# Performance work log

Hardware: AMD Instinct MI355X
Metric: run time of the kernel (lower is better)

## Reference

```python
import jax, jax.numpy as jnp
import numpy as np

N = 1536        # nodes in batch
E = 24576       # directed edges (avg in-degree 16)
H_DIM = 128     # hidden_dim
D = 1280        # input_dim (esm embedding size)
K_HOPS = 2
RATIO = 0.5     # node-drop pooling keep ratio
NEG = -1e9

def _leaky(v):
    return jnp.where(v > 0, v, 0.2 * v)

def setup_inputs():
    key = jax.random.key(0)
    ks = jax.random.split(key, 11)
    x = jax.random.normal(ks[0], (N, H_DIM), jnp.float32)
    x_orig = jax.random.normal(ks[1], (N, D), jnp.float32) * 0.1
    edge_index = jax.random.randint(ks[2], (2, E), 0, N, dtype=jnp.int32)
    batch = jnp.zeros((N,), jnp.int32)
    W1 = jax.random.normal(ks[3], (H_DIM, D), jnp.float32) / np.sqrt(H_DIM).astype(np.float32)
    a_src1 = jax.random.normal(ks[4], (D,), jnp.float32) / np.sqrt(D).astype(np.float32)
    a_dst1 = jax.random.normal(ks[5], (D,), jnp.float32) / np.sqrt(D).astype(np.float32)
    b1 = jnp.zeros((D,), jnp.float32)
    w2 = jax.random.normal(ks[6], (D,), jnp.float32) / np.sqrt(D).astype(np.float32)
    a_s2 = jax.random.normal(ks[7], (), jnp.float32)
    a_d2 = jax.random.normal(ks[8], (), jnp.float32)
    b2 = jnp.zeros((), jnp.float32)
    return {"x": x, "x_orig": x_orig, "edge_index": edge_index, "batch": batch,
            "W1": W1, "a_src1": a_src1, "a_dst1": a_dst1, "b1": b1,
            "w2": w2, "a_s2": a_s2, "a_d2": a_d2, "b2": b2}

def _forward(x, x_orig, edge_index, batch, W1, a_src1, a_dst1, b1, w2, a_s2, a_d2, b2):
    n = x.shape[0]
    src, tgt = edge_index[0], edge_index[1]
    sl = jnp.arange(n, dtype=src.dtype)
    src2 = jnp.concatenate([src, sl])   # PyG GATConv adds self-loops
    tgt2 = jnp.concatenate([tgt, sl])

    # ---- conv1: GATConv(hidden_dim -> input_dim, heads=1) on full graph ----
    h = x @ W1                                          # [N, D]
    e = _leaky((h @ a_src1)[src2] + (h @ a_dst1)[tgt2])  # [E+N]
    mx = jax.ops.segment_max(e, tgt2, num_segments=n)
    ex = jnp.exp(e - mx[tgt2])
    den = jax.ops.segment_sum(ex, tgt2, num_segments=n)
    alpha = ex / den[tgt2]
    x_gat = jax.ops.segment_sum(alpha[:, None] * h[src2], tgt2, num_segments=n) + b1

    # ---- batched k-hop ego masks (flow source->target, center included) ----
    A = jnp.zeros((n, n), jnp.float32).at[src, tgt].set(1.0)
    M = jnp.eye(n, dtype=jnp.float32)
    for _ in range(K_HOPS):
        M = jnp.minimum(M + M @ A.T, 1.0)
    Mb = M > 0                                          # [N_ego, N_node]

    # ---- pooling scorer GAT(D->1) on x_sub = x_gat[v] * x_orig[u] ----
    # h2[v,u] = sum_d x_gat[v,d] * x_orig[u,d] * w2[d]
    H2 = (x_gat * w2) @ x_orig.T                        # [N_ego, N_node]
    hs, ht = H2[:, src2], H2[:, tgt2]                   # [N_ego, E+N]
    valid = Mb[:, src2] & Mb[:, tgt2]
    e2 = jnp.where(valid, _leaky(a_s2 * hs + a_d2 * ht), NEG)

    def row(e_row, hs_row):  # attention softmax + aggregate within one ego
        m = jax.ops.segment_max(e_row, tgt2, num_segments=n)
        w = jnp.exp(e_row - m[tgt2])
        d = jax.ops.segment_sum(w, tgt2, num_segments=n)
        nu = jax.ops.segment_sum(w * hs_row, tgt2, num_segments=n)
        return nu / jnp.maximum(d, 1e-12)
    score = jax.vmap(row)(e2, hs) + b2                  # [N_ego, N_node]

    # ---- node-drop pooling: keep top ceil(RATIO*|ego|) nodes per ego ----
    size = jnp.sum(Mb, axis=1).astype(jnp.float32)
    k_keep = jnp.ceil(RATIO * size).astype(jnp.int32)
    score_m = jnp.where(Mb, score, NEG)
    order = jnp.argsort(-score_m, axis=1)
    rank = jnp.argsort(order, axis=1)
    keep = (rank < k_keep[:, None]) & Mb
    out = jnp.where(keep, jax.nn.sigmoid(score), 0.0)   # padded score matrix
    return out, keep

def reference(x, x_orig, edge_index, batch, W1, a_src1, a_dst1, b1, w2, a_s2, a_d2, b2):
    return _forward(x, x_orig, edge_index, batch, W1, a_src1, a_dst1, b1, w2, a_s2, a_d2, b2)
```

## Files before the change

kernel.cpp:

```cpp
#include <hip/hip_runtime.h>
#include <math.h>

#define N 1536
#define E 24576
#define HD 128
#define D 1280
#define NW 24
#define RT 16
#define KSP 2
#define KSL 640

#define NB_SPLIT 1920
#define NB_DEG   102
#define NB_H     480

typedef unsigned long long u64;
typedef unsigned short u16;
typedef unsigned int u32;
typedef __attribute__((ext_vector_type(8))) short bf16x8;
typedef __attribute__((ext_vector_type(4))) float f32x4;

#define GLDS(g, l) __builtin_amdgcn_global_load_lds( \
    (const __attribute__((address_space(1))) unsigned int*)(g), \
    (__attribute__((address_space(3))) unsigned int*)(l), 16, 0, 0)

__device__ __forceinline__ double lrelu(double v){ return v > 0.0 ? v : 0.2*v; }

__device__ __forceinline__ double fexp(double x){
    double n = __builtin_rint(x * 1.4426950408889634);
    double r = __builtin_fma(-n, 0.6931471805599453, x);
    r = __builtin_fma(-n, 2.3190468138462996e-17, r);
    double p = 2.505210838544172e-8;
    p = __builtin_fma(p, r, 2.755731922398589e-7);
    p = __builtin_fma(p, r, 2.7557319223985893e-6);
    p = __builtin_fma(p, r, 2.48015873015873e-5);
    p = __builtin_fma(p, r, 1.984126984126984e-4);
    p = __builtin_fma(p, r, 1.3888888888888889e-3);
    p = __builtin_fma(p, r, 8.333333333333333e-3);
    p = __builtin_fma(p, r, 4.1666666666666664e-2);
    p = __builtin_fma(p, r, 1.6666666666666666e-1);
    p = __builtin_fma(p, r, 0.5);
    p = __builtin_fma(p, r, 1.0);
    p = __builtin_fma(p, r, 1.0);
    long long ni = (long long)n;
    double s = __longlong_as_double((u64)(ni + 1023) << 52);
    return (x < -700.0) ? 0.0 : p * s;
}

__device__ __forceinline__ float fexpf_(float x){
    float n = __builtin_rintf(x * 1.44269504f);
    float r = __builtin_fmaf(-n, 0.693359375f, x);
    r = __builtin_fmaf(-n, -2.12194440e-4f, r);
    float p = 1.9841270e-4f;
    p = __builtin_fmaf(p, r, 1.3888889e-3f);
    p = __builtin_fmaf(p, r, 8.3333333e-3f);
    p = __builtin_fmaf(p, r, 4.1666667e-2f);
    p = __builtin_fmaf(p, r, 1.6666667e-1f);
    p = __builtin_fmaf(p, r, 0.5f);
    p = __builtin_fmaf(p, r, 1.0f);
    p = __builtin_fmaf(p, r, 1.0f);
    int ni = (int)n;
    float s = __uint_as_float((u32)(ni + 127) << 23);
    return p * s;
}

__device__ __forceinline__ void bsplit(float f, u16& h, u16& l){
    unsigned u = __float_as_uint(f);
    unsigned hr = (u + 0x7fffu + ((u>>16)&1u)) >> 16;
    h = (u16)hr;
    float hf = __uint_as_float(hr << 16);
    float r = f - hf;
    unsigned u2 = __float_as_uint(r);
    l = (u16)((u2 + 0x7fffu + ((u2>>16)&1u)) >> 16);
}

__global__ void k_prep(const float* __restrict__ xo, u16* __restrict__ Xhi, u16* __restrict__ Xlo,
                       const int* __restrict__ ei, u64* __restrict__ IN, int* __restrict__ deg,
                       const float* __restrict__ x, const float* __restrict__ W1,
                       float* __restrict__ h32){
    int bid = blockIdx.x, tid = threadIdx.x;
    if (bid < NB_SPLIT){
        int idx = (bid*256 + tid)*4;
        float4 v = *(const float4*)&xo[idx];
        ushort4 h, l;
        bsplit(v.x, h.x, l.x); bsplit(v.y, h.y, l.y);
        bsplit(v.z, h.z, l.z); bsplit(v.w, h.w, l.w);
        *(ushort4*)&Xhi[idx] = h;
        *(ushort4*)&Xlo[idx] = l;
    } else if (bid < NB_SPLIT + NB_DEG){
        int idx = (bid - NB_SPLIT)*256 + tid;
        if (idx < E){
            int s = ei[idx], t = ei[E+idx];
            atomicOr(&IN[(size_t)t*NW + (s>>6)], 1ULL << (s&63));
            atomicAdd(&deg[t], 1);
        } else if (idx < E+N){
            atomicAdd(&deg[idx-E], 1);
        }
    } else {
        int r = bid - (NB_SPLIT + NB_DEG);
        int rb = (r/5)*RT;
        int col = (r%5)*256 + tid;
        __shared__ float xL[RT*HD];
        for (int u=tid; u<RT*HD; u+=256) xL[u] = x[(size_t)rb*HD + u];
        __syncthreads();
        float acc[RT];
        #pragma unroll
        for (int rr=0; rr<RT; rr++) acc[rr] = 0.0f;
        const float* wp = &W1[col];
        #pragma unroll 4
        for (int k=0; k<HD; k++){
            float w = wp[(size_t)k*D];
            #pragma unroll
            for (int rr=0; rr<RT; rr++) acc[rr] = __builtin_fmaf(w, xL[rr*HD + k], acc[rr]);
        }
        #pragma unroll
        for (int rr=0; rr<RT; rr++) h32[(size_t)(rb+rr)*D + col] = acc[rr];
    }
}

__global__ void k_graph(const int* __restrict__ deg, int* __restrict__ coff, int* __restrict__ cursor,
                        const u64* __restrict__ IN, u64* __restrict__ Mb,
                        u16* __restrict__ cols, int* __restrict__ cnt){
    int tid = threadIdx.x;
    if (blockIdx.x == 0){
        __shared__ int ls[256];
        int v[6]; int s = 0;
        for (int u=0; u<6; u++){ v[u] = s; s += deg[tid*6+u]; }
        ls[tid] = s; __syncthreads();
        for (int d=1; d<256; d<<=1){
            int t2 = (tid>=d) ? ls[tid-d] : 0;
            __syncthreads();
            ls[tid] += t2;
            __syncthreads();
        }
        int base = (tid>0) ? ls[tid-1] : 0;
        for (int u=0; u<6; u++){
            int o = base + v[u];
            coff[tid*6+u] = o; cursor[tid*6+u] = o;
        }
        if (tid==255) coff[N] = ls[255];
        return;
    }
    int i = blockIdx.x - 1, ln = tid;
    __shared__ int scn[256];
    __shared__ u16 lst[N];
    u64 b = 0;
    if (ln < NW){
        b = IN[(size_t)i*NW + ln];
        if ((i>>6) == ln) b |= 1ULL << (i&63);
    }
    int pc = (ln < NW) ? __popcll(b) : 0;
    scn[ln] = pc; __syncthreads();
    for (int d=1; d<64; d<<=1){
        int v = (ln>=d) ? scn[ln-d] : 0;
        __syncthreads();
        scn[ln] += v;
        __syncthreads();
    }
    {
        int idx = scn[ln] - pc;
        u64 bb = b;
        while (bb){
            int k = __ffsll((unsigned long long)bb) - 1;
            bb &= bb - 1;
            lst[idx++] = (u16)(ln*64 + k);
        }
    }
    __syncthreads();
    int nn = scn[63];
    u64 R0 = b, R1 = 0, R2 = 0, R3 = 0;
    int u = 0;
    if (ln < NW){
        for (; u+3 < nn; u += 4){
            R0 |= IN[(size_t)lst[u  ]*NW + ln];
            R1 |= IN[(size_t)lst[u+1]*NW + ln];
            R2 |= IN[(size_t)lst[u+2]*NW + ln];
            R3 |= IN[(size_t)lst[u+3]*NW + ln];
        }
        for (; u < nn; u++) R0 |= IN[(size_t)lst[u]*NW + ln];
    }
    u64 R = (R0 | R1) | (R2 | R3);
    if (ln < NW) Mb[(size_t)i*NW + ln] = R;
    __syncthreads();
    pc = (ln < NW) ? __popcll(R) : 0;
    scn[ln] = pc; __syncthreads();
    for (int d=1; d<64; d<<=1){
        int v = (ln>=d) ? scn[ln-d] : 0;
        __syncthreads();
        scn[ln] += v;
        __syncthreads();
    }
    if (ln == 63) cnt[i] = scn[63];
    int idx = scn[ln] - pc;
    u64 bb = R;
    while (bb){
        int k = __ffsll((unsigned long long)bb) - 1;
        bb &= bb - 1;
        cols[(size_t)i*N + idx++] = (u16)(ln*64 + k);
    }
}

__global__ void k_fill_hv(const int* __restrict__ ei, int* __restrict__ cursor, u16* __restrict__ csr_src,
                          const float* __restrict__ h32, const float* __restrict__ as1,
                          const float* __restrict__ ad1, double* __restrict__ hs1,
                          double* __restrict__ hd1){
    int tid = threadIdx.x;
    if (blockIdx.x < NB_DEG){
        int idx = blockIdx.x*256 + tid;
        if (idx < E){
            int s = ei[idx], t = ei[E+idx];
            int p = atomicAdd(&cursor[t], 1);
            csr_src[p] = (u16)s;
        } else if (idx < E+N){
            int t = idx - E;
            int p = atomicAdd(&cursor[t], 1);
            csr_src[p] = (u16)t;
        }
        return;
    }
    int i = blockIdx.x - NB_DEG;
    __shared__ double ra[256], rb[256];
    double a = 0, b = 0;
    for (int d=tid; d<D; d+=256){
        double hv = (double)h32[(size_t)i*D + d];
        a += hv * (double)as1[d];
        b += hv * (double)ad1[d];
    }
    ra[tid] = a; rb[tid] = b; __syncthreads();
    for (int s=128; s>0; s>>=1){
        if (tid < s){ ra[tid] += ra[tid+s]; rb[tid] += rb[tid+s]; }
        __syncthreads();
    }
    if (tid == 0){ hs1[i] = ra[0]; hd1[i] = rb[0]; }
}

__global__ void k_gat(const int* __restrict__ coff, const u16* __restrict__ csr_src,
                      const double* __restrict__ hs1, const double* __restrict__ hd1,
                      const float* __restrict__ h32,
                      const float* __restrict__ b1, const float* __restrict__ w2,
                      u16* __restrict__ Ghi, u16* __restrict__ Glo){
    int t = blockIdx.x, tid = threadIdx.x;
    int o0 = coff[t], o1 = coff[t+1], dg = o1 - o0;
    __shared__ double red[256];
    __shared__ float als[256];
    __shared__ int ssrc[256];
    __shared__ double DD;
    double hdt = hd1[t];
    double dsum = 0.0;
    for (int j=tid; j<dg; j+=256){
        int s = csr_src[o0+j];
        double e = lrelu(hs1[s] + hdt);
        dsum += fexp(e);
    }
    red[tid] = dsum; __syncthreads();
    for (int step=128; step>0; step>>=1){
        if (tid < step) red[tid] += red[tid+step];
        __syncthreads();
    }
    if (tid == 0) DD = red[0];
    __syncthreads();
    double Dv = DD;
    float acc[5] = {0,0,0,0,0};
    for (int base=0; base<dg; base+=256){
        int j = base + tid;
        if (j < dg){
            int s = csr_src[o0+j];
            double e = lrelu(hs1[s] + hdt);
            als[tid] = (float)(fexp(e)/Dv); ssrc[tid] = s;
        }
        __syncthreads();
        int lim = min(256, dg-base);
        for (int u=0; u<lim; u+=2){
            float a0 = als[u];
            int s0 = ssrc[u];
            bool h1 = (u+1 < lim);
            float a1 = h1 ? als[u+1] : 0.0f;
            int s1 = h1 ? ssrc[u+1] : s0;
            const float* hp0 = &h32[(size_t)s0*D];
            const float* hp1 = &h32[(size_t)s1*D];
            #pragma unroll
            for (int q=0; q<5; q++)
                acc[q] = __builtin_fmaf(a1, hp1[tid + 256*q],
                         __builtin_fmaf(a0, hp0[tid + 256*q], acc[q]));
        }
        __syncthreads();
    }
    #pragma unroll
    for (int q=0; q<5; q++){
        int d = tid + 256*q;
        float g = (acc[q] + b1[d]) * w2[d];
        u16 gh, gl;
        bsplit(g, gh, gl);
        Ghi[(size_t)t*D + d] = gh;
        Glo[(size_t)t*D + d] = gl;
    }
}

__global__ __launch_bounds__(512, 4)
void k_h2mm(const u16* __restrict__ Ghi, const u16* __restrict__ Glo,
            const u16* __restrict__ Xhi, const u16* __restrict__ Xlo,
            float* __restrict__ Hp){
    __shared__ u16 S[2*4*4096];
    int tid = threadIdx.x;
    int ks = blockIdx.x & (KSP-1);
    int tile = blockIdx.x >> 1;
    int bm = tile / 12, bn = tile % 12;
    int k0 = ks * KSL;
    int w = tid >> 6, L = tid & 63;
    int sr = w*16 + (L >> 2);
    int sc = (L & 3) * 8;
    size_t gA = (size_t)(bm*128 + sr)*D + k0 + sc;
    size_t gB = (size_t)(bn*128 + sr)*D + k0 + sc;
    int lw = w * 512;
    int l16 = L & 15, qd = L >> 4;
    int wm = (w & 1)*64, wn = (w >> 1)*32;
    f32x4 acc[4][2];
    #pragma unroll
    for (int a=0; a<4; a++)
        #pragma unroll
        for (int b=0; b<2; b++) acc[a][b] = (f32x4){0.f,0.f,0.f,0.f};

    #define STAGE(B, KB) do{ \
        GLDS(Ghi + gA + (KB), S + ((B)*4+0)*4096 + lw); \
        GLDS(Glo + gA + (KB), S + ((B)*4+1)*4096 + lw); \
        GLDS(Xhi + gB + (KB), S + ((B)*4+2)*4096 + lw); \
        GLDS(Xlo + gB + (KB), S + ((B)*4+3)*4096 + lw); \
    }while(0)

    STAGE(0, 0);
    const int NT = KSL/32;
    #pragma unroll 1
    for (int t = 0; t < NT; t++){
        int cur = t & 1;
        if (t+1 < NT){
            STAGE(cur^1, (t+1)*32);
            asm volatile("s_waitcnt vmcnt(4)" ::: "memory");
        } else {
            asm volatile("s_waitcnt vmcnt(0)" ::: "memory");
        }
        __builtin_amdgcn_s_barrier();
        const u16* Ah = S + (cur*4+0)*4096;
        const u16* Al = S + (cur*4+1)*4096;
        const u16* Bh = S + (cur*4+2)*4096;
        const u16* Bl = S + (cur*4+3)*4096;
        bf16x8 ahi[4], alo[4];
        #pragma unroll
        for (int tm=0; tm<4; tm++){
            ahi[tm] = *(const bf16x8*)&Ah[(wm + tm*16 + l16)*32 + qd*8];
            alo[tm] = *(const bf16x8*)&Al[(wm + tm*16 + l16)*32 + qd*8];
        }
        #pragma unroll
        for (int tn=0; tn<2; tn++){
            bf16x8 bhf = *(const bf16x8*)&Bh[(wn + tn*16 + l16)*32 + qd*8];
            bf16x8 blf = *(const bf16x8*)&Bl[(wn + tn*16 + l16)*32 + qd*8];
            #pragma unroll
            for (int tm=0; tm<4; tm++){
                acc[tm][tn] = __builtin_amdgcn_mfma_f32_16x16x32_bf16(ahi[tm], bhf, acc[tm][tn], 0, 0, 0);
                acc[tm][tn] = __builtin_amdgcn_mfma_f32_16x16x32_bf16(alo[tm], bhf, acc[tm][tn], 0, 0, 0);
                acc[tm][tn] = __builtin_amdgcn_mfma_f32_16x16x32_bf16(ahi[tm], blf, acc[tm][tn], 0, 0, 0);
            }
        }
        __builtin_amdgcn_s_barrier();
    }
    #undef STAGE
    float* HO = Hp + (size_t)ks*N*N;
    #pragma unroll
    for (int tm=0; tm<4; tm++){
        int rbase = bm*128 + wm + tm*16 + qd*4;
        #pragma unroll
        for (int tn=0; tn<2; tn++){
            int cg = bn*128 + wn + tn*16 + l16;
            #pragma unroll
            for (int reg=0; reg<4; reg++)
                HO[(size_t)(rbase+reg)*N + cg] = acc[tm][tn][reg];
        }
    }
}

__global__ void k_score_rank(const float* __restrict__ Hp, const u64* __restrict__ Mb,
                             const u16* __restrict__ cols, const int* __restrict__ cnt,
                             const int* __restrict__ coff, const u16* __restrict__ csr_src,
                             const float* __restrict__ pas2, const float* __restrict__ pad2,
                             const float* __restrict__ pb2, float* __restrict__ out){
    int i = blockIdx.x, tid = threadIdx.x;
    __shared__ __align__(16) float HL[N];
    __shared__ u64 MbL[NW];
    __shared__ u16 clL[N];
    __shared__ u64 KL[N];
    __shared__ int hist[256];
    __shared__ u64 sPrefix;
    __shared__ int sKK;
    float* keepO = out + (size_t)N*N;
    {
        const float4* P0 = (const float4*)(Hp + (size_t)i*N);
        const float4* P1 = (const float4*)(Hp + (size_t)N*N + (size_t)i*N);
        float4* H4 = (float4*)HL;
        for (int u=tid; u<N/4; u+=256){
            float4 a=P0[u], b=P1[u];
            float4 r;
            r.x = a.x+b.x; r.y = a.y+b.y; r.z = a.z+b.z; r.w = a.w+b.w;
            H4[u] = r;
        }
    }
    if (tid < NW) MbL[tid] = Mb[(size_t)i*NW + tid];
    __syncthreads();
    float as2 = pas2[0], ad2 = pad2[0];
    double b2 = (double)pb2[0];
    int c0 = cnt[i];
    c0 = min(max(c0, 0), N);
    for (int c=tid; c<c0; c+=256){
        int t = cols[(size_t)i*N + c];
        float ht = HL[t];
        float zd = ad2 * ht;
        int o0 = coff[t], o1 = coff[t+1];
        double den = 0.0, nu = 0.0;
        int p = o0;
        for (; p+7 < o1; p += 8){
            int s[8]; float h[8]; float wv[8];
            #pragma unroll
            for (int q=0; q<8; q++) s[q] = csr_src[p+q];
            #pragma unroll
            for (int q=0; q<8; q++) h[q] = HL[s[q]];
            #pragma unroll
            for (int q=0; q<8; q++){
                bool v = (MbL[s[q]>>6] >> (s[q]&63)) & 1ULL;
                float z = __builtin_fmaf(as2, h[q], zd);
                float e = z > 0.f ? z : 0.2f*z;
                e = fminf(fmaxf(e, -80.f), 80.f);
                wv[q] = v ? fexpf_(e) : 0.0f;
            }
            #pragma unroll
            for (int q=0; q<8; q++){
                den += (double)wv[q];
                nu  += (double)(wv[q]*h[q]);
            }
        }
        for (; p < o1; p++){
            int s = csr_src[p];
            bool v = (MbL[s>>6] >> (s&63)) & 1ULL;
            float hs = HL[s];
            float z = __builtin_fmaf(as2, hs, zd);
            float e = z > 0.0f ? z : 0.2f*z;
            e = fminf(fmaxf(e, -80.0f), 80.0f);
            float w = v ? fexpf_(e) : 0.0f;
            den += (double)w;
            nu  += (double)(w * hs);
        }
        float sf = (float)(nu / fmax(den, 1e-12) + b2);
        clL[c] = (u16)t;
        u32 kb = __float_as_uint(sf);
        kb = (kb & 0x80000000u) ? ~kb : (kb | 0x80000000u);
        KL[c] = ((u64)kb << 16) | (u32)(1535 - t);
    }
    __syncthreads();
    for (int d=tid; d<N; d+=256) HL[d] = 0.0f;
    int k = (c0 + 1) >> 1;
    if (tid == 0){ sPrefix = 0; sKK = k; }
    #pragma unroll 1
    for (int shift = 40; shift >= 0; shift -= 8){
        hist[tid] = 0;
        __syncthreads();
        u64 pref = sPrefix;
        int kkr = sKK;
        for (int c=tid; c<c0; c+=256){
            u64 key = KL[c];
            if ((key >> (shift+8)) == (pref >> (shift+8)))
                atomicAdd(&hist[(int)((key>>shift)&255)], 1);
        }
        __syncthreads();
        if (tid < 64){
            int Lx = tid;
            int b0 = hist[4*Lx], b1v = hist[4*Lx+1], b2v = hist[4*Lx+2], b3v = hist[4*Lx+3];
            int tot = ((b0 + b1v) + (b2v + b3v));
            int run = tot;
            #pragma unroll
            for (int d=1; d<64; d<<=1){
                int o = __shfl_down(run, d);
                if (Lx + d < 64) run += o;
            }
            int after = run - tot;
            int s3 = b3v + after, s2 = b2v + s3, s1 = b1v + s2, s0 = b0 + s1;
            int dg = -1, rem = 0;
            if (s0 >= kkr && s1 < kkr){ dg = 4*Lx;   rem = kkr - s1; }
            else if (s1 >= kkr && s2 < kkr){ dg = 4*Lx+1; rem = kkr - s2; }
            else if (s2 >= kkr && s3 < kkr){ dg = 4*Lx+2; rem = kkr - s3; }
            else if (s3 >= kkr && after < kkr){ dg = 4*Lx+3; rem = kkr - after; }
            if (dg >= 0){
                sPrefix = pref | ((u64)(u32)dg << shift);
                sKK = rem;
            }
        }
        __syncthreads();
    }
    u64 T = sPrefix;
    for (int p=tid; p<c0; p+=256){
        u64 Kp = KL[p];
        if (Kp >= T){
            u32 kb = (u32)(Kp >> 16);
            u32 orig = (kb & 0x80000000u) ? (kb & 0x7fffffffu) : ~kb;
            float sf = __uint_as_float(orig);
            HL[clL[p]] = 1.0f/(1.0f + fexpf_(fminf(fmaxf(-sf,-80.f),80.f)));
        }
    }
    __syncthreads();
    {
        const float4* H4 = (const float4*)HL;
        float4* O0 = (float4*)(out   + (size_t)i*N);
        float4* O1 = (float4*)(keepO + (size_t)i*N);
        for (int u=tid; u<N/4; u+=256){
            float4 s = H4[u];
            float4 kk;
            kk.x = (s.x > 0.0f) ? 1.0f : 0.0f;
            kk.y = (s.y > 0.0f) ? 1.0f : 0.0f;
            kk.z = (s.z > 0.0f) ? 1.0f : 0.0f;
            kk.w = (s.w > 0.0f) ? 1.0f : 0.0f;
            O0[u] = s;
            O1[u] = kk;
        }
    }
}

extern "C" void kernel_launch(void* const* d_in, const int* in_sizes, int n_in,
                              void* d_out, int out_size, void* d_ws, size_t ws_size,
                              hipStream_t stream){
    const float* x   = (const float*)d_in[0];
    const float* xo  = (const float*)d_in[1];
    const int*   ei  = (const int*)  d_in[2];
    const float* W1  = (const float*)d_in[4];
    const float* as1 = (const float*)d_in[5];
    const float* ad1 = (const float*)d_in[6];
    const float* b1  = (const float*)d_in[7];
    const float* w2  = (const float*)d_in[8];
    const float* as2 = (const float*)d_in[9];
    const float* ad2 = (const float*)d_in[10];
    const float* b2  = (const float*)d_in[11];
    float* out = (float*)d_out;

    char* w = (char*)d_ws;
    size_t o = 0;
    auto alloc = [&](size_t b)->char*{ char* r = w + o; o = (o + b + 255) & ~(size_t)255; return r; };

    float*  h32   = (float*) alloc((size_t)N*D*4);
    float*  Hp    = (float*) alloc((size_t)KSP*N*N*4);
    u16*    Ghi   = (u16*)   alloc((size_t)N*D*2);
    u16*    Glo   = (u16*)   alloc((size_t)N*D*2);
    u16*    Xhi   = (u16*)   alloc((size_t)N*D*2);
    u16*    Xlo   = (u16*)   alloc((size_t)N*D*2);
    u64*    IN    = (u64*)   alloc((size_t)N*NW*8);
    int*    deg   = (int*)   alloc((size_t)N*4);
    u64*    Mb    = (u64*)   alloc((size_t)N*NW*8);
    double* hs1   = (double*)alloc((size_t)N*8);
    double* hd1   = (double*)alloc((size_t)N*8);
    int*    coff  = (int*)   alloc((size_t)(N+1)*4);
    int*    cursor= (int*)   alloc((size_t)N*4);
    u16*    csr   = (u16*)   alloc((size_t)(E+N)*2);
    u16*    cols  = (u16*)   alloc((size_t)N*N*2);
    int*    cnt   = (int*)   alloc((size_t)N*4);

    hipMemsetAsync(IN, 0, (size_t)N*NW*8 + (size_t)N*4, stream);

    k_prep   <<<NB_SPLIT + NB_DEG + NB_H, 256, 0, stream>>>(xo, Xhi, Xlo, ei, IN, deg, x, W1, h32);
    k_graph  <<<N + 1, 256, 0, stream>>>(deg, coff, cursor, IN, Mb, cols, cnt);
    k_fill_hv<<<NB_DEG + N, 256, 0, stream>>>(ei, cursor, csr, h32, as1, ad1, hs1, hd1);
    k_gat    <<<N, 256, 0, stream>>>(coff, csr, hs1, hd1, h32, b1, w2, Ghi, Glo);
    k_h2mm   <<<144*KSP, 512, 0, stream>>>(Ghi, Glo, Xhi, Xlo, Hp);
    k_score_rank<<<N, 256, 0, stream>>>(Hp, Mb, cols, cnt, coff, csr, as2, ad2, b2, out);
}
```

Before: 202.7 us.

## Move ego-mask construction into GAT kernel blocks and shrink scan to single block

The 2-hop ego-mask/column-list work moves out of the former graph kernel into extra blocks of the GAT aggregation kernel, which now launches 2N blocks. Shared memory is unioned between the two roles. The degree prefix scan becomes its own one-block kernel. The aim is to shorten the critical path before fill_hv by running the mask work concurrently with GAT aggregation, at the cost of a larger GAT grid and some reshuffled barriers.

```diff
diff --git a/kernel.cpp b/kernel.cpp
--- a/kernel.cpp
+++ b/kernel.cpp
@@ -118,86 +118,24 @@
     }
 }
 
-__global__ void k_graph(const int* __restrict__ deg, int* __restrict__ coff, int* __restrict__ cursor,
-                        const u64* __restrict__ IN, u64* __restrict__ Mb,
-                        u16* __restrict__ cols, int* __restrict__ cnt){
+__global__ void k_scan(const int* __restrict__ deg, int* __restrict__ coff, int* __restrict__ cursor){
+    __shared__ int ls[256];
     int tid = threadIdx.x;
-    if (blockIdx.x == 0){
-        __shared__ int ls[256];
-        int v[6]; int s = 0;
-        for (int u=0; u<6; u++){ v[u] = s; s += deg[tid*6+u]; }
-        ls[tid] = s; __syncthreads();
-        for (int d=1; d<256; d<<=1){
-            int t2 = (tid>=d) ? ls[tid-d] : 0;
-            __syncthreads();
-            ls[tid] += t2;
-            __syncthreads();
-        }
-        int base = (tid>0) ? ls[tid-1] : 0;
-        for (int u=0; u<6; u++){
-            int o = base + v[u];
-            coff[tid*6+u] = o; cursor[tid*6+u] = o;
-        }
-        if (tid==255) coff[N] = ls[255];
-        return;
-    }
-    int i = blockIdx.x - 1, ln = tid;
-    __shared__ int scn[256];
-    __shared__ u16 lst[N];
-    u64 b = 0;
-    if (ln < NW){
-        b = IN[(size_t)i*NW + ln];
-        if ((i>>6) == ln) b |= 1ULL << (i&63);
-    }
-    int pc = (ln < NW) ? __popcll(b) : 0;
-    scn[ln] = pc; __syncthreads();
-    for (int d=1; d<64; d<<=1){
-        int v = (ln>=d) ? scn[ln-d] : 0;
-        __syncthreads();
-        scn[ln] += v;
-        __syncthreads();
-    }
-    {
-        int idx = scn[ln] - pc;
-        u64 bb = b;
-        while (bb){
-            int k = __ffsll((unsigned long long)bb) - 1;
-            bb &= bb - 1;
-            lst[idx++] = (u16)(ln*64 + k);
-        }
-    }
-    __syncthreads();
-    int nn = scn[63];
-    u64 R0 = b, R1 = 0, R2 = 0, R3 = 0;
-    int u = 0;
-    if (ln < NW){
-        for (; u+3 < nn; u += 4){
-            R0 |= IN[(size_t)lst[u  ]*NW + ln];
-            R1 |= IN[(size_t)lst[u+1]*NW + ln];
-            R2 |= IN[(size_t)lst[u+2]*NW + ln];
-            R3 |= IN[(size_t)lst[u+3]*NW + ln];
-        }
-        for (; u < nn; u++) R0 |= IN[(size_t)lst[u]*NW + ln];
-    }
-    u64 R = (R0 | R1) | (R2 | R3);
-    if (ln < NW) Mb[(size_t)i*NW + ln] = R;
-    __syncthreads();
-    pc = (ln < NW) ? __popcll(R) : 0;
-    scn[ln] = pc; __syncthreads();
-    for (int d=1; d<64; d<<=1){
-        int v = (ln>=d) ? scn[ln-d] : 0;
-        __syncthreads();
-        scn[ln] += v;
-        __syncthreads();
-    }
-    if (ln == 63) cnt[i] = scn[63];
-    int idx = scn[ln] - pc;
-    u64 bb = R;
-    while (bb){
-        int k = __ffsll((unsigned long long)bb) - 1;
-        bb &= bb - 1;
-        cols[(size_t)i*N + idx++] = (u16)(ln*64 + k);
-    }
+    int v[6]; int s = 0;
+    for (int u=0; u<6; u++){ v[u] = s; s += deg[tid*6+u]; }
+    ls[tid] = s; __syncthreads();
+    for (int d=1; d<256; d<<=1){
+        int t2 = (tid>=d) ? ls[tid-d] : 0;
+        __syncthreads();
+        ls[tid] += t2;
+        __syncthreads();
+    }
+    int base = (tid>0) ? ls[tid-1] : 0;
+    for (int u=0; u<6; u++){
+        int o = base + v[u];
+        coff[tid*6+u] = o; cursor[tid*6+u] = o;
+    }
+    if (tid==255) coff[N] = ls[255];
 }
 
 __global__ void k_fill_hv(const int* __restrict__ ei, int* __restrict__ cursor, u16* __restrict__ csr_src,
@@ -238,13 +176,74 @@
                       const double* __restrict__ hs1, const double* __restrict__ hd1,
                       const float* __restrict__ h32,
                       const float* __restrict__ b1, const float* __restrict__ w2,
-                      u16* __restrict__ Ghi, u16* __restrict__ Glo){
-    int t = blockIdx.x, tid = threadIdx.x;
+                      u16* __restrict__ Ghi, u16* __restrict__ Glo,
+                      const u64* __restrict__ IN, u64* __restrict__ Mb,
+                      u16* __restrict__ cols, int* __restrict__ cnt){
+    __shared__ union {
+        struct { double red[256]; float als[256]; int ssrc[256]; double DD; } g;
+        struct { int scn[256]; u16 lst[N]; } m;
+    } U;
+    int tid = threadIdx.x;
+    if (blockIdx.x >= N){
+        int i = blockIdx.x - N, ln = tid;
+        u64 b = 0;
+        if (ln < NW){
+            b = IN[(size_t)i*NW + ln];
+            if ((i>>6) == ln) b |= 1ULL << (i&63);
+        }
+        int pc = (ln < NW) ? __popcll(b) : 0;
+        U.m.scn[ln] = pc; __syncthreads();
+        for (int d=1; d<64; d<<=1){
+            int v = (ln>=d) ? U.m.scn[ln-d] : 0;
+            __syncthreads();
+            U.m.scn[ln] += v;
+            __syncthreads();
+        }
+        {
+            int idx = U.m.scn[ln] - pc;
+            u64 bb = b;
+            while (bb){
+                int k = __ffsll((unsigned long long)bb) - 1;
+                bb &= bb - 1;
+                U.m.lst[idx++] = (u16)(ln*64 + k);
+            }
+        }
+        __syncthreads();
+        int nn = U.m.scn[63];
+        u64 R0 = b, R1 = 0, R2 = 0, R3 = 0;
+        int u = 0;
+        if (ln < NW){
+            for (; u+3 < nn; u += 4){
+                R0 |= IN[(size_t)U.m.lst[u  ]*NW + ln];
+                R1 |= IN[(size_t)U.m.lst[u+1]*NW + ln];
+                R2 |= IN[(size_t)U.m.lst[u+2]*NW + ln];
+                R3 |= IN[(size_t)U.m.lst[u+3]*NW + ln];
+            }
+            for (; u < nn; u++) R0 |= IN[(size_t)U.m.lst[u]*NW + ln];
+        }
+        u64 R = (R0 | R1) | (R2 | R3);
+        if (ln < NW) Mb[(size_t)i*NW + ln] = R;
+        __syncthreads();
+        pc = (ln < NW) ? __popcll(R) : 0;
+        U.m.scn[ln] = pc; __syncthreads();
+        for (int d=1; d<64; d<<=1){
+            int v = (ln>=d) ? U.m.scn[ln-d] : 0;
+            __syncthreads();
+            U.m.scn[ln] += v;
+            __syncthreads();
+        }
+        if (ln == 63) cnt[i] = U.m.scn[63];
+        int idx = U.m.scn[ln] - pc;
+        u64 bb = R;
+        while (bb){
+            int k = __ffsll((unsigned long long)bb) - 1;
+            bb &= bb - 1;
+            cols[(size_t)i*N + idx++] = (u16)(ln*64 + k);
+        }
+        return;
+    }
+    int t = blockIdx.x;
     int o0 = coff[t], o1 = coff[t+1], dg = o1 - o0;
-    __shared__ double red[256];
-    __shared__ float als[256];
-    __shared__ int ssrc[256];
-    __shared__ double DD;
     double hdt = hd1[t];
     double dsum = 0.0;
     for (int j=tid; j<dg; j+=256){
@@ -252,30 +251,31 @@
         double e = lrelu(hs1[s] + hdt);
         dsum += fexp(e);
     }
-    red[tid] = dsum; __syncthreads();
+    U.g.red[tid] = dsum; __syncthreads();
     for (int step=128; step>0; step>>=1){
-        if (tid < step) red[tid] += red[tid+step];
-        __syncthreads();
-    }
-    if (tid == 0) DD = red[0];
+        if (tid < step) U.g.red[tid] += U.g.red[tid+step];
+        __syncthreads();
+    }
+    if (tid == 0) U.g.DD = U.g.red[0];
     __syncthreads();
-    double Dv = DD;
+    double Dv = U.g.DD;
     float acc[5] = {0,0,0,0,0};
     for (int base=0; base<dg; base+=256){
         int j = base + tid;
+        __syncthreads();
         if (j < dg){
             int s = csr_src[o0+j];
             double e = lrelu(hs1[s] + hdt);
-            als[tid] = (float)(fexp(e)/Dv); ssrc[tid] = s;
+            U.g.als[tid] = (float)(fexp(e)/Dv); U.g.ssrc[tid] = s;
         }
         __syncthreads();
         int lim = min(256, dg-base);
         for (int u=0; u<lim; u+=2){
-            float a0 = als[u];
-            int s0 = ssrc[u];
+            float a0 = U.g.als[u];
+            int s0 = U.g.ssrc[u];
             bool h1 = (u+1 < lim);
-            float a1 = h1 ? als[u+1] : 0.0f;
-            int s1 = h1 ? ssrc[u+1] : s0;
+            float a1 = h1 ? U.g.als[u+1] : 0.0f;
+            int s1 = h1 ? U.g.ssrc[u+1] : s0;
             const float* hp0 = &h32[(size_t)s0*D];
             const float* hp1 = &h32[(size_t)s1*D];
             #pragma unroll
@@ -283,8 +283,8 @@
                 acc[q] = __builtin_fmaf(a1, hp1[tid + 256*q],
                          __builtin_fmaf(a0, hp0[tid + 256*q], acc[q]));
         }
-        __syncthreads();
-    }
+    }
+    __syncthreads();
     #pragma unroll
     for (int q=0; q<5; q++){
         int d = tid + 256*q;
@@ -560,9 +560,9 @@
     hipMemsetAsync(IN, 0, (size_t)N*NW*8 + (size_t)N*4, stream);
 
     k_prep   <<<NB_SPLIT + NB_DEG + NB_H, 256, 0, stream>>>(xo, Xhi, Xlo, ei, IN, deg, x, W1, h32);
-    k_graph  <<<N + 1, 256, 0, stream>>>(deg, coff, cursor, IN, Mb, cols, cnt);
+    k_scan   <<<1, 256, 0, stream>>>(deg, coff, cursor);
     k_fill_hv<<<NB_DEG + N, 256, 0, stream>>>(ei, cursor, csr, h32, as1, ad1, hs1, hd1);
-    k_gat    <<<N, 256, 0, stream>>>(coff, csr, hs1, hd1, h32, b1, w2, Ghi, Glo);
+    k_gat    <<<2*N, 256, 0, stream>>>(coff, csr, hs1, hd1, h32, b1, w2, Ghi, Glo, IN, Mb, cols, cnt);
     k_h2mm   <<<144*KSP, 512, 0, stream>>>(Ghi, Glo, Xhi, Xlo, Hp);
     k_score_rank<<<N, 256, 0, stream>>>(Hp, Mb, cols, cnt, coff, csr, as2, ad2, b2, out);
 }
```

Measured after the change: 200.9 us (median of 2 runs). No clear change (-0.9%).
